# Kernel tuning notes

Measured on AMD Instinct MI355X. Metric: run time of the kernel, lower is better.

The kernel has to match this reference:

```python
import jax, jax.numpy as jnp
import numpy as np

DIM_IN, DIM, BS, H, W = 128, 64, 32, 64, 64
G, K = 5, 3          # KAN grid intervals and spline degree
EPS = 1e-5           # BatchNorm eps


def conv2d(x, w, b, groups=1, pad=0):
    # x: [B,C,H,W], w: [O, C//groups, kh, kw]
    y = jax.lax.conv_general_dilated(
        x, w, window_strides=(1, 1), padding=[(pad, pad), (pad, pad)],
        dimension_numbers=('NCHW', 'OIHW', 'NCHW'), feature_group_count=groups)
    return y + b[None, :, None, None]


def bn(x, g, b, m, v):
    # inference-mode BatchNorm2d
    inv = jax.lax.rsqrt(v + EPS)
    return g[None, :, None, None] * (x - m[None, :, None, None]) * inv[None, :, None, None] + b[None, :, None, None]


def make_grid():
    # extended knot vector over [-1,1], G intervals, degree K: G+2K+1 knots
    h = 2.0 / G
    t = jnp.arange(-K, G + K + 1, dtype=jnp.float32) * h - 1.0
    return jnp.broadcast_to(t, (DIM, G + 2 * K + 1))


def bspline_basis(x, t, k):
    # Cox-de Boor recursion. x: [N,in], t: [in, G+2k+1] -> B: [N,in,G+k]
    xe = x[..., None]
    B = ((xe >= t[:, :-1]) & (xe < t[:, 1:])).astype(x.dtype)
    for p in range(1, k + 1):
        B = ((xe - t[:, :-(p + 1)]) / (t[:, p:-1] - t[:, :-(p + 1)])) * B[..., :-1] \
          + ((t[:, p + 1:] - xe) / (t[:, p + 1:] - t[:, 1:-p])) * B[..., 1:]
    return B


def kan_forward(xk, coef, scale_base, scale_sp, kan_bias):
    # single KANLayer [dim -> dim]: silu residual branch + spline branch + node bias
    t = make_grid()
    B = bspline_basis(xk, t, K)                      # [N, in, G+K]
    y_base = jax.nn.silu(xk) @ scale_base            # [N, out]
    y_sp = jnp.einsum('nij,ioj->no', B, coef * scale_sp[:, :, None])
    return y_base + y_sp + kan_bias


def setup_inputs() -> dict:
    key = jax.random.key(0)
    ks = jax.random.split(key, 24)
    rn = lambda k, s, sc=0.05: jax.random.normal(k, s, jnp.float32) * sc
    return {
        'x': jax.random.normal(ks[0], (BS, DIM_IN, H, W), jnp.float32),
        'reduce_w': rn(ks[1], (DIM, DIM_IN, 1, 1), 0.1), 'reduce_b': rn(ks[2], (DIM,)),
        'dw_w': rn(ks[3], (DIM, 1, 7, 7), 0.1), 'dw_b': rn(ks[4], (DIM,)),
        'dw_g': 1.0 + rn(ks[5], (DIM,)), 'dw_beta': rn(ks[6], (DIM,)),
        'dw_m': rn(ks[7], (DIM,)), 'dw_v': 0.5 + jax.random.uniform(ks[8], (DIM,)),
        'f2_w': rn(ks[9], (DIM, DIM, 1, 1), 0.1), 'f2_b': rn(ks[10], (DIM,)),
        'coef': rn(ks[11], (DIM, DIM, G + K), 0.1),
        'scale_base': 1.0 / np.sqrt(DIM) + rn(ks[12], (DIM, DIM)),
        'scale_sp': 1.0 + rn(ks[13], (DIM, DIM)),
        'kan_bias': rn(ks[14], (DIM,)),
        'g_w': rn(ks[15], (DIM, DIM, 1, 1), 0.1), 'g_b': rn(ks[16], (DIM,)),
        'g_g': 1.0 + rn(ks[17], (DIM,)), 'g_beta': rn(ks[18], (DIM,)),
        'g_m': rn(ks[19], (DIM,)), 'g_v': 0.5 + jax.random.uniform(ks[20], (DIM,)),
        'dw2_w': rn(ks[21], (DIM, 1, 7, 7), 0.1), 'dw2_b': rn(ks[22], (DIM,)),
    }


def reference(x, reduce_w, reduce_b, dw_w, dw_b, dw_g, dw_beta, dw_m, dw_v,
              f2_w, f2_b, coef, scale_base, scale_sp, kan_bias,
              g_w, g_b, g_g, g_beta, g_m, g_v, dw2_w, dw2_b):
    x = conv2d(x, reduce_w, reduce_b)                       # dim_reduce 1x1
    inp = x
    xd = bn(conv2d(x, dw_w, dw_b, groups=DIM, pad=3), dw_g, dw_beta, dw_m, dw_v)  # 7x7 dwconv + BN
    bs, dim, h, w = xd.shape
    xk = xd.transpose(0, 2, 3, 1).reshape(bs * h * w, dim)  # tokenwise view
    x1 = kan_forward(xk, coef, scale_base, scale_sp, kan_bias)
    x1 = x1.reshape(bs, h, w, dim).transpose(0, 3, 1, 2)    # back to NCHW
    x2 = conv2d(xd, f2_w, f2_b)                             # f2 1x1
    y = x1 * x2                                             # elementwise gate
    y = bn(conv2d(y, g_w, g_b), g_g, g_beta, g_m, g_v)      # g 1x1 + BN
    y = conv2d(y, dw2_w, dw2_b, groups=DIM, pad=3)          # dwconv2 7x7
    return inp + y
```

## Files before the change

### kernel.cpp

```cpp
#include <hip/hip_runtime.h>
#include <hip/hip_bf16.h>

#define BSZ 32
#define CIN 128
#define CD 64
#define HH 64
#define WW 64
#define PLANE (HH * WW)
#define NPIX (BSZ * HH * WW)
#define NB 8
#define BN_EPS 1e-5f

typedef __attribute__((ext_vector_type(8))) short short8v;
typedef __attribute__((ext_vector_type(4))) float f32x4;
typedef __attribute__((ext_vector_type(4))) unsigned int u32x4;

static __device__ __forceinline__ short f2bf(float f) {
    __hip_bfloat16 h = __float2bfloat16(f);
    return __builtin_bit_cast(short, h);
}
static __device__ __forceinline__ unsigned int cvtpk(float lo, float hi) {
    unsigned int r;
    asm("v_cvt_pk_bf16_f32 %0, %1, %2" : "=v"(r) : "v"(lo), "v"(hi));
    return r;
}
static __device__ __forceinline__ u32x4 basisD(float v) {
    const float tt = (v + 2.2f) * 2.5f;
    const float fi = floorf(tt);
    const int i0 = (int)fi;
    const float u = tt - fi;
    const bool inr = (tt >= 0.0f) && (tt < 11.0f);
    const float u2 = u * u, u3 = u2 * u;
    const float t1 = 1.f - u;
    const float w0 = (1.f / 6.f) * t1 * t1 * t1;
    const float w3 = (1.f / 6.f) * u3;
    const float w1 = fmaf(0.5f, u3, 2.f / 3.f) - u2;
    const float w2 = 1.f - w0 - w1 - w3;
    const unsigned W01 = cvtpk(w0, w1);
    const unsigned W23 = cvtpk(w2, w3);
    const int q0 = i0 - 3;
    int a = q0 >> 1;
    const int bpar = q0 & 1;
    if (!inr) a = 100;
    const unsigned A1c = (W01 >> 16) | (W23 << 16);
    const unsigned C0 = bpar ? (W01 << 16) : W01;
    const unsigned C1 = bpar ? A1c : W23;
    const unsigned C2 = bpar ? (W23 >> 16) : 0u;
    u32x4 D;
    D.x = (a == 0) ? C0 : (a == -1) ? C1 : (a == -2) ? C2 : 0u;
    D.y = (a == 1) ? C0 : (a == 0) ? C1 : (a == -1) ? C2 : 0u;
    D.z = (a == 2) ? C0 : (a == 1) ? C1 : (a == 0) ? C2 : 0u;
    D.w = (a == 3) ? C0 : (a == 2) ? C1 : (a == 1) ? C2 : 0u;
    return D;
}

__global__ __launch_bounds__(256) void k_prep(
    const float* __restrict__ coef, const float* __restrict__ ssp,
    const float* __restrict__ sb, const float* __restrict__ f2w,
    const float* __restrict__ reduce_w, const float* __restrict__ g_w,
    const float* __restrict__ dw_g, const float* __restrict__ dw_beta,
    const float* __restrict__ dw_m, const float* __restrict__ dw_v,
    const float* __restrict__ dw_b, const float* __restrict__ g_g,
    const float* __restrict__ g_beta, const float* __restrict__ g_m,
    const float* __restrict__ g_v, const float* __restrict__ g_b,
    short* __restrict__ W1f, short* __restrict__ W2f,
    short* __restrict__ WRf, short* __restrict__ WGf,
    float* __restrict__ cbuf)
{
    const int idx = blockIdx.x * 256 + threadIdx.x;
    if (idx < 36864) {
        const int e = idx & 7, l = (idx >> 3) & 63, c = (idx >> 9) & 3, s = idx >> 11;
        const int k = s * 32 + ((l >> 4) << 3) + e;
        const int j = (c << 4) + (l & 15);
        float v;
        if (k < 512) {
            const int i = k >> 3, t = k & 7;
            v = coef[(i * 64 + j) * 8 + t] * ssp[i * 64 + j];
        } else {
            v = sb[(k - 512) * 64 + j];
        }
        W1f[idx] = f2bf(v);
    } else if (idx < 45056) {
        const int f = idx - 36864;
        const int e = f & 7, l = (f >> 3) & 63, c = (f >> 9) & 3, s = f >> 11;
        const int k = s * 32 + ((l >> 4) << 3) + e;
        const int j = (c << 4) + (l & 15);
        W2f[f] = f2bf(f2w[j * 64 + k]);
    } else if (idx < 53248) {
        const int f = idx - 45056;
        const int e = f & 7, l = (f >> 3) & 63, c = (f >> 9) & 3, s = f >> 11;
        const int k = s * 32 + ((l >> 4) << 3) + e;
        const int j = (c << 4) + (l & 15);
        WRf[f] = f2bf(reduce_w[j * CIN + k]);
    } else if (idx < 57344) {
        const int f = idx - 53248;
        const int e = f & 7, l = (f >> 3) & 63, c = (f >> 9) & 3, s = f >> 11;
        const int k = s * 32 + ((l >> 4) << 3) + e;
        const int j = (c << 4) + (l & 15);
        WGf[f] = f2bf(g_w[j * 64 + k]);
    } else if (idx < 57600) {
        const int q = (idx - 57344) >> 6, c = idx & 63;
        if (q == 0) cbuf[c] = dw_g[c] * rsqrtf(dw_v[c] + BN_EPS);
        else if (q == 1) {
            float sc = dw_g[c] * rsqrtf(dw_v[c] + BN_EPS);
            cbuf[64 + c] = (dw_b[c] - dw_m[c]) * sc + dw_beta[c];
        } else if (q == 2) cbuf[128 + c] = g_g[c] * rsqrtf(g_v[c] + BN_EPS);
        else {
            float sc = g_g[c] * rsqrtf(g_v[c] + BN_EPS);
            cbuf[192 + c] = (g_b[c] - g_m[c]) * sc + g_beta[c];
        }
    }
}

__global__ __launch_bounds__(256) void k_reduce_mfma(
    const float* __restrict__ x, const short* __restrict__ WRf,
    const float* __restrict__ bias, float* __restrict__ out)
{
    __shared__ __align__(16) char smem[34048];
    short* As = (short*)smem;
    float* Osh = (float*)smem;
    const int bid = blockIdx.x;
    const int b = bid >> 5, h0 = (bid & 31) * 2;
    const int tid = threadIdx.x;
    const float* xb = x + (size_t)b * CIN * PLANE + h0 * WW;
#pragma unroll 1
    for (int p = 0; p < 64; ++p) {
        const int idx = tid + (p << 8);
        const int c = idx >> 7, rt = idx & 127;
        const float v = xb[(size_t)c * PLANE + rt];
        const int s = c >> 5, g = (c >> 3) & 3, e = c & 7;
        const int mt = rt >> 4, m = rt & 15;
        As[((mt * 4 + s) * 64 + (((g << 4) | m) ^ (s & 7))) * 8 + e] = f2bf(v);
    }
    __syncthreads();
    const int cw = tid >> 6, l = tid & 63;
    f32x4 acc[8];
#pragma unroll
    for (int i = 0; i < 8; ++i) acc[i] = (f32x4){0.f, 0.f, 0.f, 0.f};
#pragma unroll 1
    for (int s = 0; s < 4; ++s) {
        const short8v bfr = *(const short8v*)&WRf[((s * 4 + cw) * 64 + l) * 8];
        const int lx = l ^ (s & 7);
#pragma unroll
        for (int mt = 0; mt < 8; ++mt) {
            const short8v a = *(const short8v*)&As[((mt * 4 + s) * 64 + lx) * 8];
            acc[mt] = __builtin_amdgcn_mfma_f32_16x16x32_bf16(a, bfr, acc[mt], 0, 0, 0);
        }
    }
    __syncthreads();
    const int j = (cw << 4) + (l & 15);
    const float bj = bias[j];
    const int rb = (l >> 4) << 2;
#pragma unroll
    for (int mt = 0; mt < 8; ++mt)
#pragma unroll
        for (int r = 0; r < 4; ++r)
            Osh[j * 133 + mt * 16 + rb + r] = acc[mt][r] + bj;
    __syncthreads();
    float* ob = out + (size_t)b * CD * PLANE + h0 * WW;
#pragma unroll 1
    for (int p = 0; p < 32; ++p) {
        const int idx = tid + (p << 8);
        const int jj = idx >> 7, rt = idx & 127;
        ob[(size_t)jj * PLANE + rt] = Osh[jj * 133 + rt];
    }
}

template<bool RESID>
__global__ __launch_bounds__(256) void k_dwconv(
    const float* __restrict__ in, const float* __restrict__ filt,
    const float* __restrict__ sc, const float* __restrict__ shv,
    const float* __restrict__ resid, float* __restrict__ out)
{
    const int bid = blockIdx.x;
    const int b = bid >> 6, c4 = (bid >> 2) & 15, strip = bid & 3;
    const int H0 = strip << 4;
    const int c = c4 * 4 + (threadIdx.x >> 6);
    const int lane = threadIdx.x & 63;
    const size_t pbase = ((size_t)b * CD + c) * PLANE;
    const float* plane = in + pbase;
    const float* wp = filt + c * 49;
    float K[49];
#pragma unroll
    for (int q = 0; q < 49; ++q) K[q] = wp[q];
    const float scl = RESID ? 1.f : sc[c];
    const float shf = shv[c];
    const float* rplane = RESID ? (resid + pbase) : nullptr;
    float* oplane = out + pbase;

    float acc[7] = {0.f, 0.f, 0.f, 0.f, 0.f, 0.f, 0.f};
#pragma unroll
    for (int rr = 0; rr < 22; ++rr) {
        const int ra = H0 + rr - 3;
        float rowv = 0.f;
        if (ra >= 0 && ra < 64) rowv = plane[ra * 64 + lane];
        float sh[7];
        sh[3] = rowv;
#pragma unroll
        for (int d = 1; d <= 3; ++d) {
            float tp = __shfl(rowv, lane + d);
            sh[3 + d] = (lane + d < 64) ? tp : 0.f;
            float tm = __shfl(rowv, lane - d);
            sh[3 - d] = (lane - d >= 0) ? tm : 0.f;
        }
#pragma unroll
        for (int dy = 0; dy < 7; ++dy) {
            const int o = rr - dy;
            if (o >= 0 && o < 16) {
                const int slot = o % 7;
#pragma unroll
                for (int dx = 0; dx < 7; ++dx)
                    acc[slot] = fmaf(sh[dx], K[dy * 7 + dx], acc[slot]);
            }
        }
        const int done = rr - 6;
        if (done >= 0 && done < 16) {
            const int slot = done % 7;
            const int h = H0 + done;
            float val;
            if (RESID) val = acc[slot] + shf + rplane[h * 64 + lane];
            else       val = acc[slot] * scl + shf;
            oplane[h * 64 + lane] = val;
            acc[slot] = 0.f;
        }
    }
}

__global__ __launch_bounds__(256) void k_kan_fused(
    const float* __restrict__ xd, const short* __restrict__ W1f,
    const short* __restrict__ W2f, const short* __restrict__ WGf,
    const float* __restrict__ kb, const float* __restrict__ f2b,
    const float* __restrict__ gs, const float* __restrict__ gsh,
    float* __restrict__ z)
{
    __shared__ unsigned svS[4][1088];
    __shared__ unsigned svV[4][1088];
    const int tid = threadIdx.x;
    const int wv = tid >> 6, l = tid & 63;
    const int hi = l >> 4, m = l & 15;
    const int tg0 = blockIdx.x * 128 + wv * 32;
    const int bb = tg0 >> 12, pix0 = tg0 & 4095;
    const float* xb = xd + (size_t)bb * CD * PLANE + pix0;
    float* zb = z + (size_t)bb * CD * PLANE + pix0;
    unsigned* sS = svS[wv];
    unsigned* sV = svV[wv];

    float kbj[4], f2bj[4], sj[4], hj[4];
#pragma unroll
    for (int jt = 0; jt < 4; ++jt) {
        const int j = jt * 16 + m;
        kbj[jt] = kb[j]; f2bj[jt] = f2b[j]; sj[jt] = gs[j]; hj[jt] = gsh[j];
    }

    float xv0[16], xv1[16];
#pragma unroll
    for (int s = 0; s < 16; ++s) {
        xv0[s] = xb[(size_t)(4 * s + hi) * PLANE + m];
        xv1[s] = xb[(size_t)(4 * s + hi) * PLANE + 16 + m];
    }

    f32x4 accA0[4], accA1[4];
#pragma unroll
    for (int jt = 0; jt < 4; ++jt) {
        accA0[jt] = (f32x4){0.f, 0.f, 0.f, 0.f};
        accA1[jt] = (f32x4){0.f, 0.f, 0.f, 0.f};
    }

#pragma unroll
    for (int s = 0; s < 16; ++s) {
        const int c = 4 * s + hi;
        const float v0 = xv0[s], v1 = xv1[s];
        const float sl0 = v0 * __builtin_amdgcn_rcpf(1.0f + __expf(-v0));
        const float sl1 = v1 * __builtin_amdgcn_rcpf(1.0f + __expf(-v1));
        sS[c * 17 + m] = cvtpk(sl0, sl1);
        sV[c * 17 + m] = cvtpk(v0, v1);
        const short8v a0 = __builtin_bit_cast(short8v, basisD(v0));
        const short8v a1 = __builtin_bit_cast(short8v, basisD(v1));
#pragma unroll
        for (int jt = 0; jt < 4; ++jt) {
            const short8v bfr = *(const short8v*)&W1f[((s * 4 + jt) * 64 + l) * 8];
            accA0[jt] = __builtin_amdgcn_mfma_f32_16x16x32_bf16(a0, bfr, accA0[jt], 0, 0, 0);
            accA1[jt] = __builtin_amdgcn_mfma_f32_16x16x32_bf16(a1, bfr, accA1[jt], 0, 0, 0);
        }
    }

#pragma unroll
    for (int s2 = 0; s2 < 2; ++s2) {
        unsigned q[8];
#pragma unroll
        for (int e = 0; e < 8; ++e)
            q[e] = sS[(s2 * 32 + 8 * hi + e) * 17 + m];
        short8v f0, f1;
#pragma unroll
        for (int qi = 0; qi < 4; ++qi) {
            ((unsigned*)&f0)[qi] = (q[2 * qi] & 0xffffu) | (q[2 * qi + 1] << 16);
            ((unsigned*)&f1)[qi] = (q[2 * qi] >> 16) | (q[2 * qi + 1] & 0xffff0000u);
        }
#pragma unroll
        for (int jt = 0; jt < 4; ++jt) {
            const short8v bfr = *(const short8v*)&W1f[(((16 + s2) * 4 + jt) * 64 + l) * 8];
            accA0[jt] = __builtin_amdgcn_mfma_f32_16x16x32_bf16(f0, bfr, accA0[jt], 0, 0, 0);
            accA1[jt] = __builtin_amdgcn_mfma_f32_16x16x32_bf16(f1, bfr, accA1[jt], 0, 0, 0);
        }
    }

    f32x4 accB0[4], accB1[4];
#pragma unroll
    for (int jt = 0; jt < 4; ++jt) {
        accB0[jt] = (f32x4){0.f, 0.f, 0.f, 0.f};
        accB1[jt] = (f32x4){0.f, 0.f, 0.f, 0.f};
    }
#pragma unroll
    for (int s3 = 0; s3 < 2; ++s3) {
        unsigned q[8];
#pragma unroll
        for (int e = 0; e < 8; ++e)
            q[e] = sV[(s3 * 32 + 8 * hi + e) * 17 + m];
        short8v f0, f1;
#pragma unroll
        for (int qi = 0; qi < 4; ++qi) {
            ((unsigned*)&f0)[qi] = (q[2 * qi] & 0xffffu) | (q[2 * qi + 1] << 16);
            ((unsigned*)&f1)[qi] = (q[2 * qi] >> 16) | (q[2 * qi + 1] & 0xffff0000u);
        }
#pragma unroll
        for (int jt = 0; jt < 4; ++jt) {
            const short8v bfr = *(const short8v*)&W2f[((s3 * 4 + jt) * 64 + l) * 8];
            accB0[jt] = __builtin_amdgcn_mfma_f32_16x16x32_bf16(f0, bfr, accB0[jt], 0, 0, 0);
            accB1[jt] = __builtin_amdgcn_mfma_f32_16x16x32_bf16(f1, bfr, accB1[jt], 0, 0, 0);
        }
    }

    const int rb = hi * 4;
#pragma unroll
    for (int jt = 0; jt < 4; ++jt)
#pragma unroll
        for (int r = 0; r < 4; ++r) {
            const float ya = (accA0[jt][r] + kbj[jt]) * (accB0[jt][r] + f2bj[jt]);
            const float yb2 = (accA1[jt][r] + kbj[jt]) * (accB1[jt][r] + f2bj[jt]);
            sS[(jt * 16 + m) * 17 + rb + r] = cvtpk(ya, yb2);
        }

    f32x4 acc30[4], acc31[4];
#pragma unroll
    for (int jt = 0; jt < 4; ++jt) {
        acc30[jt] = (f32x4){0.f, 0.f, 0.f, 0.f};
        acc31[jt] = (f32x4){0.f, 0.f, 0.f, 0.f};
    }
#pragma unroll
    for (int s3 = 0; s3 < 2; ++s3) {
        unsigned q[8];
#pragma unroll
        for (int e = 0; e < 8; ++e)
            q[e] = sS[(s3 * 32 + 8 * hi + e) * 17 + m];
        short8v f0, f1;
#pragma unroll
        for (int qi = 0; qi < 4; ++qi) {
            ((unsigned*)&f0)[qi] = (q[2 * qi] & 0xffffu) | (q[2 * qi + 1] << 16);
            ((unsigned*)&f1)[qi] = (q[2 * qi] >> 16) | (q[2 * qi + 1] & 0xffff0000u);
        }
#pragma unroll
        for (int jt = 0; jt < 4; ++jt) {
            const short8v bfr = *(const short8v*)&WGf[((s3 * 4 + jt) * 64 + l) * 8];
            acc30[jt] = __builtin_amdgcn_mfma_f32_16x16x32_bf16(f0, bfr, acc30[jt], 0, 0, 0);
            acc31[jt] = __builtin_amdgcn_mfma_f32_16x16x32_bf16(f1, bfr, acc31[jt], 0, 0, 0);
        }
    }

#pragma unroll
    for (int jt = 0; jt < 4; ++jt) {
        const int j = jt * 16 + m;
        f32x4 o0, o1;
#pragma unroll
        for (int r = 0; r < 4; ++r) {
            o0[r] = acc30[jt][r] * sj[jt] + hj[jt];
            o1[r] = acc31[jt][r] * sj[jt] + hj[jt];
        }
        *(f32x4*)&zb[(size_t)j * PLANE + rb] = o0;
        *(f32x4*)&zb[(size_t)j * PLANE + 16 + rb] = o1;
    }
}

extern "C" void kernel_launch(void* const* d_in, const int* in_sizes, int n_in,
                              void* d_out, int out_size, void* d_ws, size_t ws_size,
                              hipStream_t stream)
{
    (void)in_sizes; (void)n_in; (void)out_size; (void)ws_size;
    const float* x        = (const float*)d_in[0];
    const float* reduce_w = (const float*)d_in[1];
    const float* reduce_b = (const float*)d_in[2];
    const float* dw_w     = (const float*)d_in[3];
    const float* dw_b     = (const float*)d_in[4];
    const float* dw_g     = (const float*)d_in[5];
    const float* dw_beta  = (const float*)d_in[6];
    const float* dw_m     = (const float*)d_in[7];
    const float* dw_v     = (const float*)d_in[8];
    const float* f2_w     = (const float*)d_in[9];
    const float* f2_b     = (const float*)d_in[10];
    const float* coef     = (const float*)d_in[11];
    const float* sbase    = (const float*)d_in[12];
    const float* ssp      = (const float*)d_in[13];
    const float* kbias    = (const float*)d_in[14];
    const float* g_w      = (const float*)d_in[15];
    const float* g_b      = (const float*)d_in[16];
    const float* g_g      = (const float*)d_in[17];
    const float* g_beta   = (const float*)d_in[18];
    const float* g_m      = (const float*)d_in[19];
    const float* g_v      = (const float*)d_in[20];
    const float* dw2_w    = (const float*)d_in[21];
    const float* dw2_b    = (const float*)d_in[22];
    float* out = (float*)d_out;

    const size_t NEL = (size_t)BSZ * CD * PLANE;
    short* W1f = (short*)d_ws;
    short* W2f = W1f + 36864;
    short* WRf = W2f + 8192;
    short* WGf = WRf + 8192;
    float* cbuf = (float*)((char*)d_ws + 115200);
    float* inp = (float*)((char*)d_ws + 131072);
    float* xdb = inp + NEL;
    float* z   = xdb + NEL;

    k_prep<<<225, 256, 0, stream>>>(coef, ssp, sbase, f2_w, reduce_w, g_w,
                                    dw_g, dw_beta, dw_m, dw_v, dw_b,
                                    g_g, g_beta, g_m, g_v, g_b,
                                    W1f, W2f, WRf, WGf, cbuf);
    k_reduce_mfma<<<BSZ * 32, 256, 0, stream>>>(x, WRf, reduce_b, inp);
    k_dwconv<false><<<BSZ * 16 * 4, 256, 0, stream>>>(inp, dw_w, cbuf, cbuf + 64, nullptr, xdb);
    k_kan_fused<<<NPIX / 128, 256, 0, stream>>>(xdb, W1f, W2f, WGf, kbias, f2_b,
                                                cbuf + 128, cbuf + 192, z);
    k_dwconv<true><<<BSZ * 16 * 4, 256, 0, stream>>>(z, dw2_w, nullptr, dw2_b, inp, out);
}
```

Baseline: 100.1 us.

## Use single-wave KAN blocks with register double-buffered weight and input prefetch

The fused KAN kernel now runs one 64-thread wave per block, with each block handling 32 pixels, instead of four waves per block. Shared-memory scratch shrinks to a single per-wave pad. MFMA B-fragments are prefetched two slices ahead in a register double buffer, and the input activations come through a 4-deep rolling register queue rather than all 32 values being loaded up front. The goal is to hide global-load latency behind the MFMAs and give the scheduler finer-grained occupancy, at the cost of more blocks and extra registers held for the prefetch buffers.

```diff
diff --git a/kernel.cpp b/kernel.cpp
--- a/kernel.cpp
+++ b/kernel.cpp
@@ -52,6 +52,19 @@
     D.z = (a == 2) ? C0 : (a == 1) ? C1 : (a == 0) ? C2 : 0u;
     D.w = (a == 3) ? C0 : (a == 2) ? C1 : (a == 1) ? C2 : 0u;
     return D;
+}
+static __device__ __forceinline__ void gather_frags(
+    const unsigned* __restrict__ pad, int s3, int hi, int m,
+    short8v& f0, short8v& f1)
+{
+    unsigned q[8];
+#pragma unroll
+    for (int e = 0; e < 8; ++e) q[e] = pad[(s3 * 32 + 8 * hi + e) * 17 + m];
+#pragma unroll
+    for (int qi = 0; qi < 4; ++qi) {
+        ((unsigned*)&f0)[qi] = (q[2 * qi] & 0xffffu) | (q[2 * qi + 1] << 16);
+        ((unsigned*)&f1)[qi] = (q[2 * qi] >> 16) | (q[2 * qi + 1] & 0xffff0000u);
+    }
 }
 
 __global__ __launch_bounds__(256) void k_prep(
@@ -226,24 +239,21 @@
     }
 }
 
-__global__ __launch_bounds__(256) void k_kan_fused(
+__global__ __launch_bounds__(64, 3) void k_kan_fused(
     const float* __restrict__ xd, const short* __restrict__ W1f,
     const short* __restrict__ W2f, const short* __restrict__ WGf,
     const float* __restrict__ kb, const float* __restrict__ f2b,
     const float* __restrict__ gs, const float* __restrict__ gsh,
     float* __restrict__ z)
 {
-    __shared__ unsigned svS[4][1088];
-    __shared__ unsigned svV[4][1088];
-    const int tid = threadIdx.x;
-    const int wv = tid >> 6, l = tid & 63;
+    __shared__ unsigned sS[64 * 17];
+    __shared__ unsigned sV[64 * 17];
+    const int l = threadIdx.x & 63;
     const int hi = l >> 4, m = l & 15;
-    const int tg0 = blockIdx.x * 128 + wv * 32;
+    const int tg0 = blockIdx.x * 32;
     const int bb = tg0 >> 12, pix0 = tg0 & 4095;
     const float* xb = xd + (size_t)bb * CD * PLANE + pix0;
     float* zb = z + (size_t)bb * CD * PLANE + pix0;
-    unsigned* sS = svS[wv];
-    unsigned* sV = svV[wv];
 
     float kbj[4], f2bj[4], sj[4], hj[4];
 #pragma unroll
@@ -252,11 +262,18 @@
         kbj[jt] = kb[j]; f2bj[jt] = f2b[j]; sj[jt] = gs[j]; hj[jt] = gsh[j];
     }
 
-    float xv0[16], xv1[16];
-#pragma unroll
-    for (int s = 0; s < 16; ++s) {
-        xv0[s] = xb[(size_t)(4 * s + hi) * PLANE + m];
-        xv1[s] = xb[(size_t)(4 * s + hi) * PLANE + 16 + m];
+    short8v bq[2][4];
+#pragma unroll
+    for (int jt = 0; jt < 4; ++jt)
+        bq[0][jt] = *(const short8v*)&W1f[((0 * 4 + jt) * 64 + l) * 8];
+#pragma unroll
+    for (int jt = 0; jt < 4; ++jt)
+        bq[1][jt] = *(const short8v*)&W1f[((1 * 4 + jt) * 64 + l) * 8];
+    float xq0[4], xq1[4];
+#pragma unroll
+    for (int d = 0; d < 4; ++d) {
+        xq0[d] = xb[(size_t)(4 * d + hi) * PLANE + m];
+        xq1[d] = xb[(size_t)(4 * d + hi) * PLANE + 16 + m];
     }
 
     f32x4 accA0[4], accA1[4];
@@ -268,8 +285,18 @@
 
 #pragma unroll
     for (int s = 0; s < 16; ++s) {
+        short8v cur[4];
+#pragma unroll
+        for (int jt = 0; jt < 4; ++jt) cur[jt] = bq[s & 1][jt];
+#pragma unroll
+        for (int jt = 0; jt < 4; ++jt)
+            bq[s & 1][jt] = *(const short8v*)&W1f[(((s + 2) * 4 + jt) * 64 + l) * 8];
+        const float v0 = xq0[s & 3], v1 = xq1[s & 3];
+        if (s < 12) {
+            xq0[s & 3] = xb[(size_t)(4 * (s + 4) + hi) * PLANE + m];
+            xq1[s & 3] = xb[(size_t)(4 * (s + 4) + hi) * PLANE + 16 + m];
+        }
         const int c = 4 * s + hi;
-        const float v0 = xv0[s], v1 = xv1[s];
         const float sl0 = v0 * __builtin_amdgcn_rcpf(1.0f + __expf(-v0));
         const float sl1 = v1 * __builtin_amdgcn_rcpf(1.0f + __expf(-v1));
         sS[c * 17 + m] = cvtpk(sl0, sl1);
@@ -278,29 +305,25 @@
         const short8v a1 = __builtin_bit_cast(short8v, basisD(v1));
 #pragma unroll
         for (int jt = 0; jt < 4; ++jt) {
-            const short8v bfr = *(const short8v*)&W1f[((s * 4 + jt) * 64 + l) * 8];
-            accA0[jt] = __builtin_amdgcn_mfma_f32_16x16x32_bf16(a0, bfr, accA0[jt], 0, 0, 0);
-            accA1[jt] = __builtin_amdgcn_mfma_f32_16x16x32_bf16(a1, bfr, accA1[jt], 0, 0, 0);
+            accA0[jt] = __builtin_amdgcn_mfma_f32_16x16x32_bf16(a0, cur[jt], accA0[jt], 0, 0, 0);
+            accA1[jt] = __builtin_amdgcn_mfma_f32_16x16x32_bf16(a1, cur[jt], accA1[jt], 0, 0, 0);
         }
     }
 
 #pragma unroll
     for (int s2 = 0; s2 < 2; ++s2) {
-        unsigned q[8];
-#pragma unroll
-        for (int e = 0; e < 8; ++e)
-            q[e] = sS[(s2 * 32 + 8 * hi + e) * 17 + m];
+        short8v cur[4];
+#pragma unroll
+        for (int jt = 0; jt < 4; ++jt) cur[jt] = bq[s2 & 1][jt];
+#pragma unroll
+        for (int jt = 0; jt < 4; ++jt)
+            bq[s2 & 1][jt] = *(const short8v*)&W2f[((s2 * 4 + jt) * 64 + l) * 8];
         short8v f0, f1;
-#pragma unroll
-        for (int qi = 0; qi < 4; ++qi) {
-            ((unsigned*)&f0)[qi] = (q[2 * qi] & 0xffffu) | (q[2 * qi + 1] << 16);
-            ((unsigned*)&f1)[qi] = (q[2 * qi] >> 16) | (q[2 * qi + 1] & 0xffff0000u);
-        }
+        gather_frags(sS, s2, hi, m, f0, f1);
 #pragma unroll
         for (int jt = 0; jt < 4; ++jt) {
-            const short8v bfr = *(const short8v*)&W1f[(((16 + s2) * 4 + jt) * 64 + l) * 8];
-            accA0[jt] = __builtin_amdgcn_mfma_f32_16x16x32_bf16(f0, bfr, accA0[jt], 0, 0, 0);
-            accA1[jt] = __builtin_amdgcn_mfma_f32_16x16x32_bf16(f1, bfr, accA1[jt], 0, 0, 0);
+            accA0[jt] = __builtin_amdgcn_mfma_f32_16x16x32_bf16(f0, cur[jt], accA0[jt], 0, 0, 0);
+            accA1[jt] = __builtin_amdgcn_mfma_f32_16x16x32_bf16(f1, cur[jt], accA1[jt], 0, 0, 0);
         }
     }
 
@@ -312,21 +335,18 @@
     }
 #pragma unroll
     for (int s3 = 0; s3 < 2; ++s3) {
-        unsigned q[8];
-#pragma unroll
-        for (int e = 0; e < 8; ++e)
-            q[e] = sV[(s3 * 32 + 8 * hi + e) * 17 + m];
+        short8v cur[4];
+#pragma unroll
+        for (int jt = 0; jt < 4; ++jt) cur[jt] = bq[s3 & 1][jt];
+#pragma unroll
+        for (int jt = 0; jt < 4; ++jt)
+            bq[s3 & 1][jt] = *(const short8v*)&WGf[((s3 * 4 + jt) * 64 + l) * 8];
         short8v f0, f1;
-#pragma unroll
-        for (int qi = 0; qi < 4; ++qi) {
-            ((unsigned*)&f0)[qi] = (q[2 * qi] & 0xffffu) | (q[2 * qi + 1] << 16);
-            ((unsigned*)&f1)[qi] = (q[2 * qi] >> 16) | (q[2 * qi + 1] & 0xffff0000u);
-        }
+        gather_frags(sV, s3, hi, m, f0, f1);
 #pragma unroll
         for (int jt = 0; jt < 4; ++jt) {
-            const short8v bfr = *(const short8v*)&W2f[((s3 * 4 + jt) * 64 + l) * 8];
-            accB0[jt] = __builtin_amdgcn_mfma_f32_16x16x32_bf16(f0, bfr, accB0[jt], 0, 0, 0);
-            accB1[jt] = __builtin_amdgcn_mfma_f32_16x16x32_bf16(f1, bfr, accB1[jt], 0, 0, 0);
+            accB0[jt] = __builtin_amdgcn_mfma_f32_16x16x32_bf16(f0, cur[jt], accB0[jt], 0, 0, 0);
+            accB1[jt] = __builtin_amdgcn_mfma_f32_16x16x32_bf16(f1, cur[jt], accB1[jt], 0, 0, 0);
         }
     }
 
@@ -348,21 +368,15 @@
     }
 #pragma unroll
     for (int s3 = 0; s3 < 2; ++s3) {
-        unsigned q[8];
-#pragma unroll
-        for (int e = 0; e < 8; ++e)
-            q[e] = sS[(s3 * 32 + 8 * hi + e) * 17 + m];
+        short8v cur[4];
+#pragma unroll
+        for (int jt = 0; jt < 4; ++jt) cur[jt] = bq[s3 & 1][jt];
         short8v f0, f1;
-#pragma unroll
-        for (int qi = 0; qi < 4; ++qi) {
-            ((unsigned*)&f0)[qi] = (q[2 * qi] & 0xffffu) | (q[2 * qi + 1] << 16);
-            ((unsigned*)&f1)[qi] = (q[2 * qi] >> 16) | (q[2 * qi + 1] & 0xffff0000u);
-        }
+        gather_frags(sS, s3, hi, m, f0, f1);
 #pragma unroll
         for (int jt = 0; jt < 4; ++jt) {
-            const short8v bfr = *(const short8v*)&WGf[((s3 * 4 + jt) * 64 + l) * 8];
-            acc30[jt] = __builtin_amdgcn_mfma_f32_16x16x32_bf16(f0, bfr, acc30[jt], 0, 0, 0);
-            acc31[jt] = __builtin_amdgcn_mfma_f32_16x16x32_bf16(f1, bfr, acc31[jt], 0, 0, 0);
+            acc30[jt] = __builtin_amdgcn_mfma_f32_16x16x32_bf16(f0, cur[jt], acc30[jt], 0, 0, 0);
+            acc31[jt] = __builtin_amdgcn_mfma_f32_16x16x32_bf16(f1, cur[jt], acc31[jt], 0, 0, 0);
         }
     }
 
@@ -426,7 +440,7 @@
                                     W1f, W2f, WRf, WGf, cbuf);
     k_reduce_mfma<<<BSZ * 32, 256, 0, stream>>>(x, WRf, reduce_b, inp);
     k_dwconv<false><<<BSZ * 16 * 4, 256, 0, stream>>>(inp, dw_w, cbuf, cbuf + 64, nullptr, xdb);
-    k_kan_fused<<<NPIX / 128, 256, 0, stream>>>(xdb, W1f, W2f, WGf, kbias, f2_b,
-                                                cbuf + 128, cbuf + 192, z);
+    k_kan_fused<<<NPIX / 32, 64, 0, stream>>>(xdb, W1f, W2f, WGf, kbias, f2_b,
+                                              cbuf + 128, cbuf + 192, z);
     k_dwconv<true><<<BSZ * 16 * 4, 256, 0, stream>>>(z, dw2_w, nullptr, dw2_b, inp, out);
 }
```

Measured after the change: 102.9 us. 2.8% more time.
